# Kernel optimization log

Measured on AMD Instinct MI355X. Metric: run time of the kernel, lower is better.

The kernel has to match this reference:

```python
import jax, jax.numpy as jnp
import numpy as np

B, NORM_NC, LABEL_NC, STYLE_SIZE, NHIDDEN, H, W, KS = 8, 256, 19, 512, 128, 128, 128, 3
EPS = 1e-5


def conv2d(x, w, b):
    # NCHW conv, stride 1, SAME padding (pw = ks//2)
    y = jax.lax.conv_general_dilated(x, w, window_strides=(1, 1), padding='SAME',
                                     dimension_numbers=('NCHW', 'OIHW', 'NCHW'))
    return y + b[None, :, None, None]


def setup_inputs() -> dict:
    key = jax.random.key(0)
    ks = jax.random.split(key, 16)
    s = 0.05
    return {
        'x': jax.random.normal(ks[0], (B, NORM_NC, H, W), jnp.float32),
        'segmap': jax.random.uniform(ks[1], (B, LABEL_NC, H, W), jnp.float32),
        'style': jax.random.normal(ks[2], (B, LABEL_NC, STYLE_SIZE), jnp.float32),
        'w_shared': jax.random.normal(ks[3], (NHIDDEN, LABEL_NC, KS, KS), jnp.float32) * s,
        'b_shared': jnp.zeros((NHIDDEN,), jnp.float32),
        'w_gamma': jax.random.normal(ks[4], (NORM_NC, NHIDDEN, KS, KS), jnp.float32) * s,
        'b_gamma': jnp.zeros((NORM_NC,), jnp.float32),
        'w_beta': jax.random.normal(ks[5], (NORM_NC, NHIDDEN, KS, KS), jnp.float32) * s,
        'b_beta': jnp.zeros((NORM_NC,), jnp.float32),
        'w_sgamma': jax.random.normal(ks[6], (NORM_NC, STYLE_SIZE, KS, KS), jnp.float32) * s,
        'b_sgamma': jnp.zeros((NORM_NC,), jnp.float32),
        'w_sbeta': jax.random.normal(ks[7], (NORM_NC, STYLE_SIZE, KS, KS), jnp.float32) * s,
        'b_sbeta': jnp.zeros((NORM_NC,), jnp.float32),
        'alpha_beta': jax.random.uniform(ks[8], (1,), jnp.float32),
        'alpha_gamma': jax.random.uniform(ks[9], (1,), jnp.float32),
    }


def reference(x, segmap, style, w_shared, b_shared, w_gamma, b_gamma, w_beta, b_beta,
              w_sgamma, b_sgamma, w_sbeta, b_sbeta, alpha_beta, alpha_gamma):
    # InstanceNorm2d (affine=False): per-(b,c) normalization over HxW, biased var
    mean = jnp.mean(x, axis=(2, 3), keepdims=True)
    var = jnp.var(x, axis=(2, 3), keepdims=True)
    normalized = (x - mean) * jax.lax.rsqrt(var + EPS)

    # segmap already at fm_size == out_size -> nearest interpolate is identity
    actv = jax.nn.relu(conv2d(segmap, w_shared, b_shared))  # (B, nhidden, H, W)

    # fused per-pixel contraction over label channels:
    # (style[b,l,s] * segmap[b,l,h,w]).sum(l) -> (B, style_size, H, W)
    style_map = jnp.einsum('bls,blhw->bshw', style, segmap)

    gamma = conv2d(actv, w_gamma, b_gamma)
    beta = conv2d(actv, w_beta, b_beta)
    gamma_style = conv2d(style_map, w_sgamma, b_sgamma)
    beta_style = conv2d(style_map, w_sbeta, b_sbeta)

    wb = jax.nn.sigmoid(alpha_beta)[0]
    wg = jax.nn.sigmoid(alpha_gamma)[0]
    combined_offset = wb * beta_style + (1.0 - wb) * beta
    combined_scale = wg * gamma_style + (1.0 - wg) * gamma + 1.0
    return normalized * combined_scale + combined_offset
```

## Files before the change

kernel.cpp:

```cpp
#include <hip/hip_runtime.h>
#include <hip/hip_bf16.h>
#include <cstdint>

#define B_ 8
#define LABEL_NC 19
#define H_ 128
#define W_ 128
#define UC 640
#define EPS_ 1e-5f

typedef __attribute__((ext_vector_type(8))) short s8v;
typedef __attribute__((ext_vector_type(4))) float f4v;
typedef __attribute__((ext_vector_type(4))) int i4v;
typedef unsigned short ushort_t;

__device__ __forceinline__ ushort_t f2b(float f) {
    union { float f; uint32_t u; } a; a.f = f;
    uint32_t u = a.u;
    return (ushort_t)((u + 0x7FFFu + ((u >> 16) & 1u)) >> 16);
}

__device__ __forceinline__ void gl2lds16(const ushort_t* g, ushort_t* l) {
    __builtin_amdgcn_global_load_lds(
        (const __attribute__((address_space(1))) unsigned int*)g,
        (__attribute__((address_space(3))) unsigned int*)l, 16, 0, 0);
}

__global__ void __launch_bounds__(256) k_aux(
    const float* __restrict__ x,
    const float* __restrict__ segmap, const float* __restrict__ style,
    const float* __restrict__ w_shared, const float* __restrict__ b_shared,
    const float* __restrict__ w_gamma, const float* __restrict__ w_beta,
    const float* __restrict__ w_sgamma, const float* __restrict__ w_sbeta,
    const float* __restrict__ b_gamma, const float* __restrict__ b_beta,
    const float* __restrict__ b_sgamma, const float* __restrict__ b_sbeta,
    const float* __restrict__ alpha_beta, const float* __restrict__ alpha_gamma,
    ushort_t* __restrict__ U, ushort_t* __restrict__ Wt,
    float* __restrict__ mean, float* __restrict__ rstd,
    float* __restrict__ bias_s, float* __restrict__ bias_o,
    float* __restrict__ zpage)
{
    __shared__ float seg[3][LABEL_NC][W_];
    int bid = blockIdx.x;

    if (bid < 1024) {
        int b = bid >> 7, h = bid & 127;
        const float* segb = segmap + (size_t)b * (LABEL_NC * H_ * W_);
        for (int idx = threadIdx.x; idx < 3 * LABEL_NC * W_; idx += 256) {
            int w = idx & 127;
            int l = (idx >> 7) % LABEL_NC;
            int rr = idx / (LABEL_NC * W_);
            int hh = h + rr - 1;
            seg[rr][l][w] = (hh >= 0 && hh < H_) ? segb[((size_t)l * H_ + hh) * W_ + w] : 0.f;
        }
        __syncthreads();

        int t = threadIdx.x;
        int w = t & 127;
        int grp = __builtin_amdgcn_readfirstlane(t >> 7);
        ushort_t* Urow = U + (((size_t)(b * H_ + h)) * W_ + w) * UC;

        union pack16 { ushort_t u[16]; i4v v[2]; };

        for (int cb = 0; cb < 4; ++cb) {
            int co0 = grp * 64 + cb * 16;
            float acc[16];
            #pragma unroll
            for (int i = 0; i < 16; ++i) acc[i] = b_shared[co0 + i];
            for (int l = 0; l < LABEL_NC; ++l) {
                #pragma unroll
                for (int kh = 0; kh < 3; ++kh) {
                    float sm = (w > 0)   ? seg[kh][l][w - 1] : 0.f;
                    float s0 = seg[kh][l][w];
                    float sp = (w < 127) ? seg[kh][l][w + 1] : 0.f;
                    const float* wp = w_shared + ((size_t)co0 * LABEL_NC + l) * 9 + kh * 3;
                    #pragma unroll
                    for (int i = 0; i < 16; ++i) {
                        const float* wpi = wp + i * (LABEL_NC * 9);
                        acc[i] += sm * wpi[0] + s0 * wpi[1] + sp * wpi[2];
                    }
                }
            }
            pack16 pk;
            #pragma unroll
            for (int i = 0; i < 16; ++i) pk.u[i] = f2b(acc[i] > 0.f ? acc[i] : 0.f);
            *(i4v*)(Urow + co0) = pk.v[0];
            *(i4v*)(Urow + co0 + 8) = pk.v[1];
        }

        float segr[LABEL_NC];
        #pragma unroll
        for (int l = 0; l < LABEL_NC; ++l) segr[l] = seg[1][l][w];
        const float* styb = style + (size_t)b * (LABEL_NC * 512);
        for (int sb = 0; sb < 16; ++sb) {
            int s0 = grp * 256 + sb * 16;
            float acc[16];
            #pragma unroll
            for (int i = 0; i < 16; ++i) acc[i] = 0.f;
            for (int l = 0; l < LABEL_NC; ++l) {
                const float* sp = styb + l * 512 + s0;
                float sl = segr[l];
                #pragma unroll
                for (int i = 0; i < 16; ++i) acc[i] += sl * sp[i];
            }
            pack16 pk;
            #pragma unroll
            for (int i = 0; i < 16; ++i) pk.u[i] = f2b(acc[i]);
            *(i4v*)(Urow + 128 + s0) = pk.v[0];
            *(i4v*)(Urow + 128 + s0 + 8) = pk.v[1];
        }
    } else if (bid < 3072) {
        int bc = bid - 1024;
        const float4* p = (const float4*)(x + (size_t)bc * (H_ * W_));
        float s = 0.f, s2 = 0.f;
        for (int i = threadIdx.x; i < H_ * W_ / 4; i += 256) {
            float4 v = p[i];
            s += v.x + v.y + v.z + v.w;
            s2 += v.x * v.x + v.y * v.y + v.z * v.z + v.w * v.w;
        }
        #pragma unroll
        for (int o = 32; o > 0; o >>= 1) { s += __shfl_xor(s, o); s2 += __shfl_xor(s2, o); }
        __shared__ float red[8];
        int wave = threadIdx.x >> 6, lane = threadIdx.x & 63;
        if (lane == 0) { red[wave] = s; red[wave + 4] = s2; }
        __syncthreads();
        if (threadIdx.x == 0) {
            float ts = red[0] + red[1] + red[2] + red[3];
            float t2 = red[4] + red[5] + red[6] + red[7];
            float m = ts * (1.f / 16384.f);
            float v = t2 * (1.f / 16384.f) - m * m;
            mean[bc] = m;
            rstd[bc] = rsqrtf(v + EPS_);
        }
    } else {
        float wb = 1.f / (1.f + __expf(-alpha_beta[0]));
        float wg = 1.f / (1.f + __expf(-alpha_gamma[0]));
        int gid = (bid - 3072) * 256 + threadIdx.x;
        if (gid < 256) bias_s[gid] = wg * b_sgamma[gid] + (1.f - wg) * b_gamma[gid];
        else if (gid < 512) bias_o[gid - 256] = wb * b_sbeta[gid - 256] + (1.f - wb) * b_beta[gid - 256];
        if (gid < 8192) zpage[gid] = 0.f;

        const int total = 9 * 512 * 640;
        for (int idx = gid; idx < total; idx += 2048 * 256) {
            int tap = idx / (512 * 640);
            int r = idx - tap * (512 * 640);
            int co = r / 640, ci = r - co * 640;
            int kh = tap / 3, kw = tap - kh * 3;
            float v;
            if (co < 256) {
                if (ci < 128) v = (1.f - wg) * w_gamma[((co * 128 + ci) * 3 + kh) * 3 + kw];
                else          v = wg * w_sgamma[((co * 512 + (ci - 128)) * 3 + kh) * 3 + kw];
            } else {
                int c2 = co - 256;
                if (ci < 128) v = (1.f - wb) * w_beta[((c2 * 128 + ci) * 3 + kh) * 3 + kw];
                else          v = wb * w_sbeta[((c2 * 512 + (ci - 128)) * 3 + kh) * 3 + kw];
            }
            Wt[idx] = f2b(v);
        }
    }
}

#define BK 32

__global__ void __launch_bounds__(512, 1) k_conv(
    const ushort_t* __restrict__ U, const ushort_t* __restrict__ Wt,
    const ushort_t* __restrict__ zp,
    const float* __restrict__ x, const float* __restrict__ mean, const float* __restrict__ rstd,
    const float* __restrict__ bias_s, const float* __restrict__ bias_o,
    float* __restrict__ out)
{
    int orig = blockIdx.x;
    int wg = (orig & 7) * 128 + (orig >> 3);
    int mtile = wg >> 1;
    int cohalf = wg & 1;
    int b = mtile >> 6;
    int h0 = (mtile & 63) << 1;

    extern __shared__ ushort_t smem[];

    int t = threadIdx.x;
    int wv = t >> 6, ln = t & 63;
    int wm = wv >> 1, wn = wv & 1;

    const ushort_t* Ub = U + (size_t)b * (H_ * W_ * UC);

    f4v acc[4][8] = {};

    auto stage_A = [&](int ci0, int ab) {
        ushort_t* sAb = smem + ab * 16384;
        #pragma unroll
        for (int i = 0; i < 4; ++i) {
            int issue = wv * 4 + i;
            int hh = h0 - 1 + (issue >> 3);
            int w = issue * 16 + (ln >> 2);
            int sl = (ln & 3) ^ ((w >> 1) & 3);
            const ushort_t* src = (hh >= 0 && hh < H_)
                ? Ub + ((size_t)hh * W_ + (w & 127)) * UC + ci0 + (sl << 3)
                : zp + (size_t)ln * 8;
            gl2lds16(src, sAb + (size_t)issue * 512);
        }
    };
    auto stage_B = [&](int tapX, int ci0X, int bi) {
        ushort_t* base = smem + 32768 + bi * 8192;
        #pragma unroll
        for (int j = 0; j < 2; ++j) {
            int issue = wv * 2 + j;
            int c = issue * 16 + (ln >> 2);
            int sl = (ln & 3) ^ ((c >> 1) & 3);
            int gq = (c >> 6) & 1;
            int cbase = ((c >> 7) << 6) + (c & 63);
            int co = gq * 256 + cohalf * 128 + cbase;
            const ushort_t* src = Wt + ((size_t)tapX * 512 + co) * UC + ci0X + (sl << 3);
            gl2lds16(src, base + (size_t)issue * 512);
        }
    };

    stage_A(0, 0);
    stage_B(0, 0, 0);
    stage_B(1, 0, 1);

    for (int ch = 0; ch < 20; ++ch) {
        int ci0 = ch * BK;
        ushort_t* sAb = smem + (ch & 1) * 16384;
        bool lastch = (ch == 19);
        #pragma unroll
        for (int tap = 0; tap < 9; ++tap) {
            const int dhp1 = tap / 3;
            const int dw = tap - dhp1 * 3 - 1;
            const int bi = tap % 3;
            const int bi2 = (tap + 2) % 3;

            if (tap == 8) {
                if (lastch) { asm volatile("s_waitcnt vmcnt(0)" ::: "memory"); }
                else        { asm volatile("s_waitcnt vmcnt(6)" ::: "memory"); }
            } else          { asm volatile("s_waitcnt vmcnt(2)" ::: "memory"); }
            __builtin_amdgcn_s_barrier();

            if (tap < 7)        stage_B(tap + 2, ci0, bi2);
            else if (!lastch) {
                if (tap == 7) { stage_B(0, ci0 + BK, bi2); stage_A(ci0 + BK, (ch + 1) & 1); }
                else          stage_B(1, ci0 + BK, bi2);
            }

            ushort_t* sBb = smem + 32768 + bi * 8192;
            int sd = ln >> 4;
            s8v af[4];
            #pragma unroll
            for (int mi = 0; mi < 4; ++mi) {
                int p = wm * 64 + mi * 16 + (ln & 15);
                int q = (p & 127) + dw;
                int qc = q < 0 ? 0 : (q > 127 ? 127 : q);
                int r = (p >> 7) + dhp1;
                s8v v = *(const s8v*)&sAb[(size_t)(((r * 128 + qc) << 2) + (sd ^ ((qc >> 1) & 3))) * 8];
                if (dw != 0 && (q < 0 || q > 127)) { s8v z = {}; v = z; }
                af[mi] = v;
            }
            s8v bf[8];
            #pragma unroll
            for (int ni = 0; ni < 8; ++ni) {
                int c = wn * 128 + (ni >> 2) * 64 + (ni & 3) * 16 + (ln & 15);
                bf[ni] = *(const s8v*)&sBb[(size_t)((c << 2) + (sd ^ ((c >> 1) & 3))) * 8];
            }
            __builtin_amdgcn_s_setprio(1);
            #pragma unroll
            for (int mi = 0; mi < 4; ++mi)
                #pragma unroll
                for (int ni = 0; ni < 8; ++ni)
                    acc[mi][ni] = __builtin_amdgcn_mfma_f32_16x16x32_bf16(
                        af[mi], bf[ni], acc[mi][ni], 0, 0, 0);
            __builtin_amdgcn_s_setprio(0);
        }
    }

    int bc_base = b * 256;
    #pragma unroll
    for (int ni = 0; ni < 4; ++ni) {
        int chn = cohalf * 128 + wn * 64 + ni * 16 + (ln & 15);
        float bs = bias_s[chn] + 1.f;
        float bo = bias_o[chn];
        float mu = mean[bc_base + chn];
        float rs = rstd[bc_base + chn];
        #pragma unroll
        for (int mi = 0; mi < 4; ++mi) {
            #pragma unroll
            for (int r = 0; r < 4; ++r) {
                int p = wm * 64 + mi * 16 + ((ln >> 4) << 2) + r;
                int hh = h0 + (p >> 7);
                int ww = p & 127;
                size_t xi = (((size_t)(bc_base + chn)) * H_ + hh) * W_ + ww;
                float xn = (x[xi] - mu) * rs;
                out[xi] = xn * (acc[mi][ni][r] + bs) + (acc[mi][ni + 4][r] + bo);
            }
        }
    }
}

extern "C" void kernel_launch(void* const* d_in, const int* in_sizes, int n_in,
                              void* d_out, int out_size, void* d_ws, size_t ws_size,
                              hipStream_t stream)
{
    const float* x        = (const float*)d_in[0];
    const float* segmap   = (const float*)d_in[1];
    const float* style    = (const float*)d_in[2];
    const float* w_shared = (const float*)d_in[3];
    const float* b_shared = (const float*)d_in[4];
    const float* w_gamma  = (const float*)d_in[5];
    const float* b_gamma  = (const float*)d_in[6];
    const float* w_beta   = (const float*)d_in[7];
    const float* b_beta   = (const float*)d_in[8];
    const float* w_sgamma = (const float*)d_in[9];
    const float* b_sgamma = (const float*)d_in[10];
    const float* w_sbeta  = (const float*)d_in[11];
    const float* b_sbeta  = (const float*)d_in[12];
    const float* alpha_beta  = (const float*)d_in[13];
    const float* alpha_gamma = (const float*)d_in[14];
    float* out = (float*)d_out;

    char* ws = (char*)d_ws;
    float*    ws_mean  = (float*)(ws + 0);
    float*    ws_rstd  = (float*)(ws + 8192);
    float*    ws_bs    = (float*)(ws + 16384);
    float*    ws_bo    = (float*)(ws + 18432);
    ushort_t* ws_Wt    = (ushort_t*)(ws + 20480);
    ushort_t* ws_zp    = (ushort_t*)(ws + 6 * 1024 * 1024 - 65536);
    ushort_t* ws_U     = (ushort_t*)(ws + 6 * 1024 * 1024);

    (void)hipFuncSetAttribute((const void*)k_conv,
                              hipFuncAttributeMaxDynamicSharedMemorySize, 114688);

    k_aux<<<dim3(5120), dim3(256), 0, stream>>>(x, segmap, style, w_shared, b_shared,
                                                w_gamma, w_beta, w_sgamma, w_sbeta,
                                                b_gamma, b_beta, b_sgamma, b_sbeta,
                                                alpha_beta, alpha_gamma,
                                                ws_U, ws_Wt, ws_mean, ws_rstd,
                                                ws_bs, ws_bo, (float*)ws_zp);
    k_conv<<<dim3(1024), dim3(512), 114688, stream>>>(ws_U, ws_Wt, ws_zp, x, ws_mean, ws_rstd,
                                                      ws_bs, ws_bo, out);
}
```

Baseline: 924.6 us.

## Shrink conv tile to one row and 128 channels, running two blocks per CU

Each conv block now computes one output row (128 pixels) against 64 gamma plus 64 beta channels with 256 threads. The previous block covered two rows and 128+128 channels with 512 threads. The grid grows from 1024 to 4096 blocks, and shared memory drops to 72KB so two blocks can be resident per CU, aiming for better latency hiding and load balance. In exchange, halo reuse falls: three input rows are staged per output row instead of four per two. LDS fragment reads per MFMA also roughly double, and the accumulator count per thread is halved.

```diff
diff --git a/kernel.cpp b/kernel.cpp
--- a/kernel.cpp
+++ b/kernel.cpp
@@ -162,7 +162,7 @@
 
 #define BK 32
 
-__global__ void __launch_bounds__(512, 1) k_conv(
+__global__ void __launch_bounds__(256, 2) k_conv(
     const ushort_t* __restrict__ U, const ushort_t* __restrict__ Wt,
     const ushort_t* __restrict__ zp,
     const float* __restrict__ x, const float* __restrict__ mean, const float* __restrict__ rstd,
@@ -170,46 +170,46 @@
     float* __restrict__ out)
 {
     int orig = blockIdx.x;
-    int wg = (orig & 7) * 128 + (orig >> 3);
-    int mtile = wg >> 1;
-    int cohalf = wg & 1;
-    int b = mtile >> 6;
-    int h0 = (mtile & 63) << 1;
+    int wg = (orig & 7) * 512 + (orig >> 3);
+    int mrow = wg >> 2;
+    int chq = wg & 3;
+    int b = mrow >> 7;
+    int h = mrow & 127;
 
     extern __shared__ ushort_t smem[];
 
     int t = threadIdx.x;
     int wv = t >> 6, ln = t & 63;
     int wm = wv >> 1, wn = wv & 1;
+    int sd = ln >> 4;
 
     const ushort_t* Ub = U + (size_t)b * (H_ * W_ * UC);
 
-    f4v acc[4][8] = {};
+    f4v acc[4][4] = {};
 
     auto stage_A = [&](int ci0, int ab) {
-        ushort_t* sAb = smem + ab * 16384;
-        #pragma unroll
-        for (int i = 0; i < 4; ++i) {
-            int issue = wv * 4 + i;
-            int hh = h0 - 1 + (issue >> 3);
-            int w = issue * 16 + (ln >> 2);
+        ushort_t* sAb = smem + ab * 12288;
+        #pragma unroll
+        for (int i = 0; i < 6; ++i) {
+            int issue = wv * 6 + i;
+            int rr = issue >> 3;
+            int hh = h - 1 + rr;
+            int w = (issue & 7) * 16 + (ln >> 2);
             int sl = (ln & 3) ^ ((w >> 1) & 3);
             const ushort_t* src = (hh >= 0 && hh < H_)
-                ? Ub + ((size_t)hh * W_ + (w & 127)) * UC + ci0 + (sl << 3)
+                ? Ub + ((size_t)hh * W_ + w) * UC + ci0 + (sl << 3)
                 : zp + (size_t)ln * 8;
             gl2lds16(src, sAb + (size_t)issue * 512);
         }
     };
     auto stage_B = [&](int tapX, int ci0X, int bi) {
-        ushort_t* base = smem + 32768 + bi * 8192;
+        ushort_t* base = smem + 24576 + bi * 4096;
         #pragma unroll
         for (int j = 0; j < 2; ++j) {
             int issue = wv * 2 + j;
             int c = issue * 16 + (ln >> 2);
             int sl = (ln & 3) ^ ((c >> 1) & 3);
-            int gq = (c >> 6) & 1;
-            int cbase = ((c >> 7) << 6) + (c & 63);
-            int co = gq * 256 + cohalf * 128 + cbase;
+            int co = ((c >> 6) << 8) + chq * 64 + (c & 63);
             const ushort_t* src = Wt + ((size_t)tapX * 512 + co) * UC + ci0X + (sl << 3);
             gl2lds16(src, base + (size_t)issue * 512);
         }
@@ -221,7 +221,7 @@
 
     for (int ch = 0; ch < 20; ++ch) {
         int ci0 = ch * BK;
-        ushort_t* sAb = smem + (ch & 1) * 16384;
+        ushort_t* sAb = smem + (ch & 1) * 12288;
         bool lastch = (ch == 19);
         #pragma unroll
         for (int tap = 0; tap < 9; ++tap) {
@@ -232,7 +232,7 @@
 
             if (tap == 8) {
                 if (lastch) { asm volatile("s_waitcnt vmcnt(0)" ::: "memory"); }
-                else        { asm volatile("s_waitcnt vmcnt(6)" ::: "memory"); }
+                else        { asm volatile("s_waitcnt vmcnt(8)" ::: "memory"); }
             } else          { asm volatile("s_waitcnt vmcnt(2)" ::: "memory"); }
             __builtin_amdgcn_s_barrier();
 
@@ -242,30 +242,29 @@
                 else          stage_B(1, ci0 + BK, bi2);
             }
 
-            ushort_t* sBb = smem + 32768 + bi * 8192;
-            int sd = ln >> 4;
             s8v af[4];
             #pragma unroll
             for (int mi = 0; mi < 4; ++mi) {
                 int p = wm * 64 + mi * 16 + (ln & 15);
-                int q = (p & 127) + dw;
+                int q = p + dw;
                 int qc = q < 0 ? 0 : (q > 127 ? 127 : q);
-                int r = (p >> 7) + dhp1;
-                s8v v = *(const s8v*)&sAb[(size_t)(((r * 128 + qc) << 2) + (sd ^ ((qc >> 1) & 3))) * 8];
+                s8v v = *(const s8v*)&sAb[(size_t)(((dhp1 * 128 + qc) << 2) + (sd ^ ((qc >> 1) & 3))) * 8];
                 if (dw != 0 && (q < 0 || q > 127)) { s8v z = {}; v = z; }
                 af[mi] = v;
             }
-            s8v bf[8];
-            #pragma unroll
-            for (int ni = 0; ni < 8; ++ni) {
-                int c = wn * 128 + (ni >> 2) * 64 + (ni & 3) * 16 + (ln & 15);
+            ushort_t* sBb = smem + 24576 + bi * 4096;
+            s8v bf[4];
+            #pragma unroll
+            for (int ni = 0; ni < 4; ++ni) {
+                int c = ((ni >> 1) << 6) + wn * 32 + (ni & 1) * 16 + (ln & 15);
                 bf[ni] = *(const s8v*)&sBb[(size_t)((c << 2) + (sd ^ ((c >> 1) & 3))) * 8];
             }
+
             __builtin_amdgcn_s_setprio(1);
             #pragma unroll
             for (int mi = 0; mi < 4; ++mi)
                 #pragma unroll
-                for (int ni = 0; ni < 8; ++ni)
+                for (int ni = 0; ni < 4; ++ni)
                     acc[mi][ni] = __builtin_amdgcn_mfma_f32_16x16x32_bf16(
                         af[mi], bf[ni], acc[mi][ni], 0, 0, 0);
             __builtin_amdgcn_s_setprio(0);
@@ -274,8 +273,8 @@
 
     int bc_base = b * 256;
     #pragma unroll
-    for (int ni = 0; ni < 4; ++ni) {
-        int chn = cohalf * 128 + wn * 64 + ni * 16 + (ln & 15);
+    for (int ni = 0; ni < 2; ++ni) {
+        int chn = chq * 64 + wn * 32 + ni * 16 + (ln & 15);
         float bs = bias_s[chn] + 1.f;
         float bo = bias_o[chn];
         float mu = mean[bc_base + chn];
@@ -285,11 +284,9 @@
             #pragma unroll
             for (int r = 0; r < 4; ++r) {
                 int p = wm * 64 + mi * 16 + ((ln >> 4) << 2) + r;
-                int hh = h0 + (p >> 7);
-                int ww = p & 127;
-                size_t xi = (((size_t)(bc_base + chn)) * H_ + hh) * W_ + ww;
+                size_t xi = (((size_t)(bc_base + chn)) * H_ + h) * W_ + p;
                 float xn = (x[xi] - mu) * rs;
-                out[xi] = xn * (acc[mi][ni][r] + bs) + (acc[mi][ni + 4][r] + bo);
+                out[xi] = xn * (acc[mi][ni][r] + bs) + (acc[mi][ni + 2][r] + bo);
             }
         }
     }
@@ -326,7 +323,7 @@
     ushort_t* ws_U     = (ushort_t*)(ws + 6 * 1024 * 1024);
 
     (void)hipFuncSetAttribute((const void*)k_conv,
-                              hipFuncAttributeMaxDynamicSharedMemorySize, 114688);
+                              hipFuncAttributeMaxDynamicSharedMemorySize, 73728);
 
     k_aux<<<dim3(5120), dim3(256), 0, stream>>>(x, segmap, style, w_shared, b_shared,
                                                 w_gamma, w_beta, w_sgamma, w_sbeta,
@@ -334,6 +331,6 @@
                                                 alpha_beta, alpha_gamma,
                                                 ws_U, ws_Wt, ws_mean, ws_rstd,
                                                 ws_bs, ws_bo, (float*)ws_zp);
-    k_conv<<<dim3(1024), dim3(512), 114688, stream>>>(ws_U, ws_Wt, ws_zp, x, ws_mean, ws_rstd,
-                                                      ws_bs, ws_bo, out);
-}
+    k_conv<<<dim3(4096), dim3(256), 73728, stream>>>(ws_U, ws_Wt, ws_zp, x, ws_mean, ws_rstd,
+                                                     ws_bs, ws_bo, out);
+}
```

Result: slower. 1.041 ms (+12.6%).

## Switch main conv GEMM to 32x32x16 MFMA with precomputed LDS indices

Applied to the files above, without the earlier changes.

Replaces the 16x16x32 bf16 MFMA tiling with 32x32x16 MFMAs (2x4 tiles of 16-wide accumulators, two k-steps per tap). This reduces LDS fragment reads per MFMA and instruction count. LDS and global source addresses are precomputed once outside the loop instead of being recomputed per tap. The epilogue now uses float4 loads and stores of x/out to match the new accumulator layout. It risks higher register pressure and changes the boundary zeroing logic to per-lane flags.

```diff
diff --git a/kernel.cpp b/kernel.cpp
--- a/kernel.cpp
+++ b/kernel.cpp
@@ -10,7 +10,7 @@
 #define EPS_ 1e-5f
 
 typedef __attribute__((ext_vector_type(8))) short s8v;
-typedef __attribute__((ext_vector_type(4))) float f4v;
+typedef __attribute__((ext_vector_type(16))) float f16v;
 typedef __attribute__((ext_vector_type(4))) int i4v;
 typedef unsigned short ushort_t;
 
@@ -184,35 +184,70 @@
 
     const ushort_t* Ub = U + (size_t)b * (H_ * W_ * UC);
 
-    f4v acc[4][8] = {};
+    f16v acc[2][4] = {};
+
+    int aidx[3][2][2];
+    #pragma unroll
+    for (int dwi = 0; dwi < 3; ++dwi)
+        #pragma unroll
+        for (int mi = 0; mi < 2; ++mi) {
+            int p = wm * 64 + mi * 32 + (ln & 31);
+            int px = p & 127;
+            int rb = p >> 7;
+            int q = px + dwi - 1;
+            int qc = q < 0 ? 0 : (q > 127 ? 127 : q);
+            #pragma unroll
+            for (int ks = 0; ks < 2; ++ks) {
+                int slot = (ks * 2 + (ln >> 5)) ^ ((qc >> 1) & 3);
+                aidx[dwi][mi][ks] = ((rb * 128 + qc) << 2) + slot;
+            }
+        }
+    int bidx[4][2];
+    #pragma unroll
+    for (int ni = 0; ni < 4; ++ni) {
+        int c = wn * 128 + ni * 32 + (ln & 31);
+        #pragma unroll
+        for (int ks = 0; ks < 2; ++ks)
+            bidx[ni][ks] = (c << 2) + ((ks * 2 + (ln >> 5)) ^ ((c >> 1) & 3));
+    }
+    bool zlo = ((wm & 1) == 0) && ((ln & 31) == 0);
+    bool zhi = ((wm & 1) == 1) && ((ln & 31) == 31);
+
+    const ushort_t* pA[4];
+    #pragma unroll
+    for (int i = 0; i < 4; ++i) {
+        int issue = wv * 4 + i;
+        int hh = h0 - 1 + (issue >> 3);
+        int w = issue * 16 + (ln >> 2);
+        int sl = (ln & 3) ^ ((w >> 1) & 3);
+        pA[i] = (hh >= 0 && hh < H_)
+            ? Ub + ((size_t)hh * W_ + (w & 127)) * UC + (sl << 3)
+            : zp + (size_t)ln * 8;
+    }
+    const ushort_t* pB[2];
+    #pragma unroll
+    for (int j = 0; j < 2; ++j) {
+        int issue = wv * 2 + j;
+        int c = issue * 16 + (ln >> 2);
+        int sl = (ln & 3) ^ ((c >> 1) & 3);
+        int gq = (c >> 6) & 1;
+        int cbase = ((c >> 7) << 6) + (c & 63);
+        int co = gq * 256 + cohalf * 128 + cbase;
+        pB[j] = Wt + (size_t)co * UC + (sl << 3);
+    }
 
     auto stage_A = [&](int ci0, int ab) {
         ushort_t* sAb = smem + ab * 16384;
         #pragma unroll
-        for (int i = 0; i < 4; ++i) {
-            int issue = wv * 4 + i;
-            int hh = h0 - 1 + (issue >> 3);
-            int w = issue * 16 + (ln >> 2);
-            int sl = (ln & 3) ^ ((w >> 1) & 3);
-            const ushort_t* src = (hh >= 0 && hh < H_)
-                ? Ub + ((size_t)hh * W_ + (w & 127)) * UC + ci0 + (sl << 3)
-                : zp + (size_t)ln * 8;
-            gl2lds16(src, sAb + (size_t)issue * 512);
-        }
+        for (int i = 0; i < 4; ++i)
+            gl2lds16(pA[i] + ci0, sAb + (size_t)(wv * 4 + i) * 512);
     };
     auto stage_B = [&](int tapX, int ci0X, int bi) {
         ushort_t* base = smem + 32768 + bi * 8192;
-        #pragma unroll
-        for (int j = 0; j < 2; ++j) {
-            int issue = wv * 2 + j;
-            int c = issue * 16 + (ln >> 2);
-            int sl = (ln & 3) ^ ((c >> 1) & 3);
-            int gq = (c >> 6) & 1;
-            int cbase = ((c >> 7) << 6) + (c & 63);
-            int co = gq * 256 + cohalf * 128 + cbase;
-            const ushort_t* src = Wt + ((size_t)tapX * 512 + co) * UC + ci0X + (sl << 3);
-            gl2lds16(src, base + (size_t)issue * 512);
-        }
+        size_t off = (size_t)tapX * (512 * UC) + ci0X;
+        #pragma unroll
+        for (int j = 0; j < 2; ++j)
+            gl2lds16(pB[j] + off, base + (size_t)(wv * 2 + j) * 512);
     };
 
     stage_A(0, 0);
@@ -226,7 +261,7 @@
         #pragma unroll
         for (int tap = 0; tap < 9; ++tap) {
             const int dhp1 = tap / 3;
-            const int dw = tap - dhp1 * 3 - 1;
+            const int dwi = tap % 3;
             const int bi = tap % 3;
             const int bi2 = (tap + 2) % 3;
 
@@ -243,53 +278,53 @@
             }
 
             ushort_t* sBb = smem + 32768 + bi * 8192;
-            int sd = ln >> 4;
-            s8v af[4];
-            #pragma unroll
-            for (int mi = 0; mi < 4; ++mi) {
-                int p = wm * 64 + mi * 16 + (ln & 15);
-                int q = (p & 127) + dw;
-                int qc = q < 0 ? 0 : (q > 127 ? 127 : q);
-                int r = (p >> 7) + dhp1;
-                s8v v = *(const s8v*)&sAb[(size_t)(((r * 128 + qc) << 2) + (sd ^ ((qc >> 1) & 3))) * 8];
-                if (dw != 0 && (q < 0 || q > 127)) { s8v z = {}; v = z; }
-                af[mi] = v;
-            }
-            s8v bf[8];
-            #pragma unroll
-            for (int ni = 0; ni < 8; ++ni) {
-                int c = wn * 128 + (ni >> 2) * 64 + (ni & 3) * 16 + (ln & 15);
-                bf[ni] = *(const s8v*)&sBb[(size_t)((c << 2) + (sd ^ ((c >> 1) & 3))) * 8];
-            }
-            __builtin_amdgcn_s_setprio(1);
-            #pragma unroll
-            for (int mi = 0; mi < 4; ++mi)
-                #pragma unroll
-                for (int ni = 0; ni < 8; ++ni)
-                    acc[mi][ni] = __builtin_amdgcn_mfma_f32_16x16x32_bf16(
-                        af[mi], bf[ni], acc[mi][ni], 0, 0, 0);
-            __builtin_amdgcn_s_setprio(0);
+            #pragma unroll
+            for (int ks = 0; ks < 2; ++ks) {
+                s8v af[2], bf[4];
+                #pragma unroll
+                for (int mi = 0; mi < 2; ++mi)
+                    af[mi] = *(const s8v*)&sAb[(size_t)(aidx[dwi][mi][ks] + dhp1 * 512) * 8];
+                if (dwi == 0) { if (zlo) { s8v z = {}; af[0] = z; } }
+                if (dwi == 2) { if (zhi) { s8v z = {}; af[1] = z; } }
+                #pragma unroll
+                for (int ni = 0; ni < 4; ++ni)
+                    bf[ni] = *(const s8v*)&sBb[(size_t)bidx[ni][ks] * 8];
+
+                __builtin_amdgcn_s_setprio(1);
+                #pragma unroll
+                for (int mi = 0; mi < 2; ++mi)
+                    #pragma unroll
+                    for (int ni = 0; ni < 4; ++ni)
+                        acc[mi][ni] = __builtin_amdgcn_mfma_f32_32x32x16_bf16(
+                            af[mi], bf[ni], acc[mi][ni], 0, 0, 0);
+                __builtin_amdgcn_s_setprio(0);
+            }
         }
     }
 
     int bc_base = b * 256;
     #pragma unroll
-    for (int ni = 0; ni < 4; ++ni) {
-        int chn = cohalf * 128 + wn * 64 + ni * 16 + (ln & 15);
+    for (int ni = 0; ni < 2; ++ni) {
+        int chn = cohalf * 128 + wn * 64 + ni * 32 + (ln & 31);
         float bs = bias_s[chn] + 1.f;
         float bo = bias_o[chn];
         float mu = mean[bc_base + chn];
         float rs = rstd[bc_base + chn];
         #pragma unroll
-        for (int mi = 0; mi < 4; ++mi) {
-            #pragma unroll
-            for (int r = 0; r < 4; ++r) {
-                int p = wm * 64 + mi * 16 + ((ln >> 4) << 2) + r;
-                int hh = h0 + (p >> 7);
-                int ww = p & 127;
+        for (int mi = 0; mi < 2; ++mi) {
+            #pragma unroll
+            for (int rg = 0; rg < 4; ++rg) {
+                int p4 = wm * 64 + mi * 32 + rg * 8 + ((ln >> 5) << 2);
+                int hh = h0 + (p4 >> 7);
+                int ww = p4 & 127;
                 size_t xi = (((size_t)(bc_base + chn)) * H_ + hh) * W_ + ww;
-                float xn = (x[xi] - mu) * rs;
-                out[xi] = xn * (acc[mi][ni][r] + bs) + (acc[mi][ni + 4][r] + bo);
+                float4 xv = *(const float4*)&x[xi];
+                float4 ov;
+                ov.x = (xv.x - mu) * rs * (acc[mi][ni][rg * 4 + 0] + bs) + (acc[mi][ni + 2][rg * 4 + 0] + bo);
+                ov.y = (xv.y - mu) * rs * (acc[mi][ni][rg * 4 + 1] + bs) + (acc[mi][ni + 2][rg * 4 + 1] + bo);
+                ov.z = (xv.z - mu) * rs * (acc[mi][ni][rg * 4 + 2] + bs) + (acc[mi][ni + 2][rg * 4 + 2] + bo);
+                ov.w = (xv.w - mu) * rs * (acc[mi][ni][rg * 4 + 3] + bs) + (acc[mi][ni + 2][rg * 4 + 3] + bo);
+                *(float4*)&out[xi] = ov;
             }
         }
     }
```

Result: slower. 1.007 ms (+8.9%).
